# Kernel tuning notes

Measured on AMD Instinct MI355X. Metric: run time of the kernel, lower is better.

## Reference

```python
import jax, jax.numpy as jnp
import numpy as np

B, S, D = 16, 2048, 128

def setup_inputs() -> dict:
    key = jax.random.key(0)
    k1, k2, k3, k4 = jax.random.split(key, 4)
    q = jax.random.normal(k1, (B, S, D), dtype=jnp.float32)
    k = jax.random.normal(k2, (B, S, D), dtype=jnp.float32)
    v = jax.random.normal(k3, (B, S, D), dtype=jnp.float32)
    scale = jnp.float32(1.0 / np.sqrt(D))
    attn_mask = jax.random.randint(k4, (B, S, S), 0, 2).astype(jnp.bool_)
    return {"q": q, "k": k, "v": v, "scale": scale, "attn_mask": attn_mask}

def reference(q, k, v, scale, attn_mask):
    # attention scores: [B, Sq, Sk]
    scores = jnp.einsum('bqd,bkd->bqk', q, k) * scale
    # masked_fill(attn_mask, -inf): True positions are masked out
    scores = jnp.where(attn_mask, -jnp.inf, scores)
    attention = jax.nn.softmax(scores, axis=2)
    # dropout prob = 0.0 -> identity
    context = jnp.einsum('bqk,bkd->bqd', attention, v)
    return (context, attention)
```

## Files before the change

### kernel.cpp

```cpp
#include <hip/hip_runtime.h>
#include <hip/hip_bf16.h>
#include <hip/hip_fp16.h>

#define B_ 16
#define S_ 2048
#define D_ 128
#define QB 64
#define KT 64
#define NT_ 32
#define LOG2E 1.4426950408889634f

typedef __attribute__((ext_vector_type(8))) short short8;
typedef __attribute__((ext_vector_type(4))) float f32x4;
typedef __attribute__((ext_vector_type(4))) float f32x4v;
typedef __attribute__((ext_vector_type(4))) int i32x4;
typedef __attribute__((ext_vector_type(4))) unsigned short u16x4;

__device__ __forceinline__ float exp2fast(float x) {
  return __builtin_amdgcn_exp2f(x);
}
__device__ __forceinline__ unsigned short f2bf(float f) {
  unsigned int u = __builtin_bit_cast(unsigned int, f);
  unsigned int r = (u + 0x7fffu + ((u >> 16) & 1u)) >> 16;
  return (unsigned short)r;
}
__device__ __forceinline__ float bf2f(unsigned short h) {
  return __builtin_bit_cast(float, (unsigned int)h << 16);
}
__device__ __forceinline__ void gl16(const void* g, void* l) {
  __builtin_amdgcn_global_load_lds(
      (const __attribute__((address_space(1))) unsigned int*)g,
      (__attribute__((address_space(3))) unsigned int*)l, 16, 0, 0);
}
__device__ __forceinline__ int swz_bid(int bid, int nwg) {
  int cpx = nwg >> 3;
  return (bid & 7) * cpx + (bid >> 3);
}

__global__ void cvt_bf16_kernel(const float* __restrict__ x,
                                unsigned short* __restrict__ y,
                                const float* __restrict__ sc, float postmul,
                                int n4) {
  int i = blockIdx.x * blockDim.x + threadIdx.x;
  if (i >= n4) return;
  float s = (sc ? sc[0] : 1.0f) * postmul;
  float4 f = reinterpret_cast<const float4*>(x)[i];
  u16x4 o;
  o[0] = f2bf(f.x * s); o[1] = f2bf(f.y * s);
  o[2] = f2bf(f.z * s); o[3] = f2bf(f.w * s);
  reinterpret_cast<u16x4*>(y)[i] = o;
}

__global__ void vtrans_kernel(const float* __restrict__ v,
                              unsigned short* __restrict__ vT) {
  __shared__ float tile[32][33];
  int b = blockIdx.z, kt = blockIdx.x, dt = blockIdx.y;
  int t = threadIdx.x;
  int c = t & 31, r0 = t >> 5;
  const float* src = v + ((size_t)b * S_ + (size_t)kt * 32) * D_ + dt * 32;
#pragma unroll
  for (int i = 0; i < 4; i++) {
    int r = r0 + 8 * i;
    tile[r][c] = src[(size_t)r * D_ + c];
  }
  __syncthreads();
  unsigned short* dst = vT + ((size_t)b * D_ + dt * 32) * S_ + (size_t)kt * 32;
#pragma unroll
  for (int i = 0; i < 4; i++) {
    int r = r0 + 8 * i;
    dst[(size_t)r * S_ + c] = f2bf(tile[c][r]);
  }
}

__global__ __launch_bounds__(512, 4)
void attn_main_kernel(const unsigned short* __restrict__ qbf,
                      const unsigned short* __restrict__ kbf,
                      const unsigned short* __restrict__ vTb,
                      const void* __restrict__ maskp,
                      float* __restrict__ ctx,
                      float* __restrict__ att) {
  __shared__ __align__(16) char kbuf[2][KT * 256];
  __shared__ __align__(16) char vbuf[2][D_ * 128];
  __shared__ __align__(16) char etile[QB * 128];
  __shared__ float zpart[8][2][16];
  __shared__ float iz_l[QB];

  const int tid = threadIdx.x;
  const int bid = swz_bid(blockIdx.x, B_ * (S_ / QB));
  const int b  = bid >> 5;
  const int q0 = (bid & 31) << 6;

  const int w   = tid >> 6;
  const int l   = tid & 63;
  const int l16 = l & 15;
  const int lq  = l >> 4;
  const int qh  = w & 1;
  const int kq  = w >> 1;

  const char* kbb = reinterpret_cast<const char*>(kbf + (((size_t)b * S_) << 7));
  const char* vbb = reinterpret_cast<const char*>(vTb + ((size_t)b * D_) * S_);

  const int krow_g = w * 4 + (l >> 4);
  const size_t ksrc = (size_t)krow_g * 256 + (((l & 15) * 16) ^ ((krow_g & 15) << 4));
  const int vrow_g = w * 8 + (l >> 3);
  const size_t vsrc = (size_t)vrow_g * (S_ * 2) + (((l & 7) * 16) ^ ((vrow_g & 7) << 4));
  const int ldsoff = w * 1024;

  gl16(kbb + ksrc,        &kbuf[0][0] + ldsoff);
  gl16(kbb + ksrc + 8192, &kbuf[0][0] + ldsoff + 8192);

  int myv = 0;
  if (tid < 256) myv = (reinterpret_cast<const unsigned int*>(maskp)[tid] > 1u) ? 1 : 0;
  const int mask_is_byte = __syncthreads_or(myv);

  short8 qf[2][4];
#pragma unroll
  for (int qg = 0; qg < 2; ++qg) {
    const unsigned short* qp =
        qbf + (((size_t)(b * S_ + q0 + qh * 32 + qg * 16 + l16)) << 7) + lq * 8;
#pragma unroll
    for (int ks = 0; ks < 4; ks++)
      qf[qg][ks] = *reinterpret_cast<const short8*>(qp + ks * 32);
  }

  const unsigned char* mask8 = reinterpret_cast<const unsigned char*>(maskp);
  const int* mask32 = reinterpret_cast<const int*>(maskp);
  size_t mrowq[2];
#pragma unroll
  for (int qg = 0; qg < 2; ++qg)
    mrowq[qg] = ((size_t)b * S_ + q0 + qh * 32 + qg * 16 + l16) * S_ + kq * 16 + lq * 4;

  unsigned int mbits[8] = {0, 0, 0, 0, 0, 0, 0, 0};
  float Zl[2] = {0.0f, 0.0f};
  const int krow_f = kq * 16 + l16;
  const int kfx = (krow_f & 15) << 4;

  for (int t = 0; t < NT_; ++t) {
    const int cur = t & 1;
    if (t < NT_ - 1) {
      const char* src = kbb + (size_t)(t + 1) * (KT * 256);
      gl16(src + ksrc,        &kbuf[cur ^ 1][0] + ldsoff);
      gl16(src + ksrc + 8192, &kbuf[cur ^ 1][0] + ldsoff + 8192);
    }
    unsigned int nib[2];
    if (mask_is_byte) {
#pragma unroll
      for (int qg = 0; qg < 2; ++qg) {
        unsigned int mv = *reinterpret_cast<const unsigned int*>(
            mask8 + mrowq[qg] + t * KT);
        nib[qg] = ((mv & 0x000000ffu) ? 1u : 0u) | ((mv & 0x0000ff00u) ? 2u : 0u) |
                  ((mv & 0x00ff0000u) ? 4u : 0u) | ((mv & 0xff000000u) ? 8u : 0u);
      }
    } else {
#pragma unroll
      for (int qg = 0; qg < 2; ++qg) {
        i32x4 mi = *reinterpret_cast<const i32x4*>(mask32 + mrowq[qg] + t * KT);
        nib[qg] = (mi[0] ? 1u : 0u) | (mi[1] ? 2u : 0u) |
                  (mi[2] ? 4u : 0u) | (mi[3] ? 8u : 0u);
      }
    }
    mbits[t >> 2] |= (nib[0] | (nib[1] << 4)) << ((t & 3) * 8);

    const char* kp = &kbuf[cur][0] + krow_f * 256;
    f32x4 a0 = {0.f, 0.f, 0.f, 0.f}, a1 = {0.f, 0.f, 0.f, 0.f};
    __builtin_amdgcn_s_setprio(1);
#pragma unroll
    for (int ks = 0; ks < 4; ++ks) {
      short8 kfr = *reinterpret_cast<const short8*>(kp + ((ks * 64 + lq * 16) ^ kfx));
      a0 = __builtin_amdgcn_mfma_f32_16x16x32_bf16(kfr, qf[0][ks], a0, 0, 0, 0);
      a1 = __builtin_amdgcn_mfma_f32_16x16x32_bf16(kfr, qf[1][ks], a1, 0, 0, 0);
    }
    __builtin_amdgcn_s_setprio(0);
#pragma unroll
    for (int r = 0; r < 4; ++r) {
      if (!((nib[0] >> r) & 1u)) Zl[0] += exp2fast(a0[r]);
      if (!((nib[1] >> r) & 1u)) Zl[1] += exp2fast(a1[r]);
    }
    __syncthreads();
  }

  gl16(kbb + ksrc,          &kbuf[0][0] + ldsoff);
  gl16(kbb + ksrc + 8192,   &kbuf[0][0] + ldsoff + 8192);
  gl16(vbb + vsrc,          &vbuf[0][0] + ldsoff);
  gl16(vbb + vsrc + 262144, &vbuf[0][0] + ldsoff + 8192);
#pragma unroll
  for (int qg = 0; qg < 2; ++qg) {
    Zl[qg] += __shfl_xor(Zl[qg], 16, 64);
    Zl[qg] += __shfl_xor(Zl[qg], 32, 64);
  }
  if (lq == 0) { zpart[w][0][l16] = Zl[0]; zpart[w][1][l16] = Zl[1]; }
  __syncthreads();
  if (tid < QB) {
    const int qh_ = tid >> 5, qg_ = (tid >> 4) & 1, r_ = tid & 15;
    float Z = 0.0f;
#pragma unroll
    for (int kk = 0; kk < 4; ++kk) Z += zpart[kk * 2 + qh_][qg_][r_];
    iz_l[tid] = 1.0f / Z;
  }
  __syncthreads();

  const float izq0 = iz_l[qh * 32 + l16];
  const float izq1 = iz_l[qh * 32 + 16 + l16];

  f32x4 apv[2][2] = {{{0.f,0.f,0.f,0.f},{0.f,0.f,0.f,0.f}},
                     {{0.f,0.f,0.f,0.f},{0.f,0.f,0.f,0.f}}};
  for (int t = 0; t < NT_; ++t) {
    const int cur = t & 1;
    if (t < NT_ - 1) {
      const char* src = kbb + (size_t)(t + 1) * (KT * 256);
      gl16(src + ksrc,        &kbuf[cur ^ 1][0] + ldsoff);
      gl16(src + ksrc + 8192, &kbuf[cur ^ 1][0] + ldsoff + 8192);
    }
    const char* kp = &kbuf[cur][0] + krow_f * 256;
    f32x4 a0 = {0.f, 0.f, 0.f, 0.f}, a1 = {0.f, 0.f, 0.f, 0.f};
    __builtin_amdgcn_s_setprio(1);
#pragma unroll
    for (int ks = 0; ks < 4; ++ks) {
      short8 kfr = *reinterpret_cast<const short8*>(kp + ((ks * 64 + lq * 16) ^ kfx));
      a0 = __builtin_amdgcn_mfma_f32_16x16x32_bf16(kfr, qf[0][ks], a0, 0, 0, 0);
      a1 = __builtin_amdgcn_mfma_f32_16x16x32_bf16(kfr, qf[1][ks], a1, 0, 0, 0);
    }
    __builtin_amdgcn_s_setprio(0);
    const unsigned int nibs = mbits[t >> 2] >> ((t & 3) * 8);
    u16x4 eb[2];
#pragma unroll
    for (int r = 0; r < 4; ++r) {
      eb[0][r] = f2bf((nibs & (1u << r)) ? 0.0f : exp2fast(a0[r]) * izq0);
      eb[1][r] = f2bf((nibs & (16u << r)) ? 0.0f : exp2fast(a1[r]) * izq1);
    }
    __syncthreads();
#pragma unroll
    for (int qg = 0; qg < 2; ++qg) {
      const int re = qh * 32 + qg * 16 + l16;
      *reinterpret_cast<u16x4*>(
          etile + re * 128 + ((kq * 32 + lq * 8) ^ ((re & 7) << 4))) = eb[qg];
    }
    __syncthreads();
#pragma unroll
    for (int h = 0; h < 2; ++h) {
      const int re = w * 8 + h * 4 + (l >> 4);
      u16x4 ev = *reinterpret_cast<const u16x4*>(
          etile + re * 128 + (((l & 15) * 8) ^ ((re & 7) << 4)));
      f32x4v pv;
#pragma unroll
      for (int j = 0; j < 4; ++j) pv[j] = bf2f(ev[j]);
      __builtin_nontemporal_store(pv, reinterpret_cast<f32x4v*>(
          att + ((size_t)(b * S_ + q0 + re)) * S_ + t * KT + (l & 15) * 4));
    }
#pragma unroll
    for (int kk = 0; kk < 2; ++kk) {
      short8 afr[2], bfr[2];
#pragma unroll
      for (int qg = 0; qg < 2; ++qg) {
        const int re = qh * 32 + qg * 16 + l16;
        afr[qg] = *reinterpret_cast<const short8*>(
            etile + re * 128 + ((kk * 64 + lq * 16) ^ ((re & 7) << 4)));
      }
#pragma unroll
      for (int dg = 0; dg < 2; ++dg) {
        const int vr = kq * 32 + dg * 16 + l16;
        bfr[dg] = *reinterpret_cast<const short8*>(
            &vbuf[cur][0] + vr * 128 + ((kk * 64 + lq * 16) ^ ((vr & 7) << 4)));
      }
      __builtin_amdgcn_s_setprio(1);
#pragma unroll
      for (int qg = 0; qg < 2; ++qg)
#pragma unroll
        for (int dg = 0; dg < 2; ++dg)
          apv[qg][dg] = __builtin_amdgcn_mfma_f32_16x16x32_bf16(
              afr[qg], bfr[dg], apv[qg][dg], 0, 0, 0);
      __builtin_amdgcn_s_setprio(0);
    }
    if (t < NT_ - 1) {
      const char* vs2 = vbb + (size_t)(t + 1) * 128;
      gl16(vs2 + vsrc,          &vbuf[cur ^ 1][0] + ldsoff);
      gl16(vs2 + vsrc + 262144, &vbuf[cur ^ 1][0] + ldsoff + 8192);
    }
  }

#pragma unroll
  for (int qg = 0; qg < 2; ++qg) {
#pragma unroll
    for (int dg = 0; dg < 2; ++dg) {
#pragma unroll
      for (int r = 0; r < 4; ++r) {
        __builtin_nontemporal_store(
            apv[qg][dg][r],
            ctx + ((size_t)(b * S_ + q0 + qh * 32 + qg * 16 + lq * 4 + r)) * D_ +
                kq * 32 + dg * 16 + l16);
      }
    }
  }
}

extern "C" void kernel_launch(void* const* d_in, const int* in_sizes, int n_in,
                              void* d_out, int out_size, void* d_ws, size_t ws_size,
                              hipStream_t stream) {
  (void)in_sizes; (void)n_in; (void)out_size; (void)ws_size;
  const float* q = (const float*)d_in[0];
  const float* k = (const float*)d_in[1];
  const float* v = (const float*)d_in[2];
  const float* scale = (const float*)d_in[3];
  const void* mask = d_in[4];

  const size_t qkv_elems = (size_t)B_ * S_ * D_;
  unsigned short* qbf = (unsigned short*)d_ws;
  unsigned short* kbf = qbf + qkv_elems;
  unsigned short* vTb = kbf + qkv_elems;

  float* ctx = (float*)d_out;
  float* att = ctx + (size_t)B_ * S_ * D_;

  const int n4 = B_ * S_ * D_ / 4;
  cvt_bf16_kernel<<<dim3((n4 + 255) / 256), dim3(256), 0, stream>>>(
      q, qbf, scale, LOG2E, n4);
  cvt_bf16_kernel<<<dim3((n4 + 255) / 256), dim3(256), 0, stream>>>(
      k, kbf, nullptr, 1.0f, n4);
  vtrans_kernel<<<dim3(S_ / 32, D_ / 32, B_), dim3(256), 0, stream>>>(v, vTb);
  attn_main_kernel<<<dim3(B_ * (S_ / QB)), dim3(512), 0, stream>>>(
      qbf, kbf, vTb, mask, ctx, att);
}
```

Baseline: 159.9 us.

## Halve key tile to 32 and remap warps for higher occupancy

Shrinks the key tile from 64 to 32 columns, which doubles the iteration count and halves the LDS buffers for K, V and the probability tile. Warps are remapped so each handles 16 query rows and half of the key/D range instead of 32 rows. Launch bounds ask for 8 blocks per CU so more waves can hide latency. The cost is twice as many barriers per pass, less MFMA reuse per K fragment, and narrower mask and attention-output stores per iteration.

Result: slower. 250.3 us (+56.5%).

```diff
diff --git a/kernel.cpp b/kernel.cpp
--- a/kernel.cpp
+++ b/kernel.cpp
@@ -6,8 +6,8 @@
 #define S_ 2048
 #define D_ 128
 #define QB 64
-#define KT 64
-#define NT_ 32
+#define KT 32
+#define NT_ 64
 #define LOG2E 1.4426950408889634f
 
 typedef __attribute__((ext_vector_type(8))) short short8;
@@ -72,7 +72,7 @@
   }
 }
 
-__global__ __launch_bounds__(512, 4)
+__global__ __launch_bounds__(512, 8)
 void attn_main_kernel(const unsigned short* __restrict__ qbf,
                       const unsigned short* __restrict__ kbf,
                       const unsigned short* __restrict__ vTb,
@@ -80,9 +80,9 @@
                       float* __restrict__ ctx,
                       float* __restrict__ att) {
   __shared__ __align__(16) char kbuf[2][KT * 256];
-  __shared__ __align__(16) char vbuf[2][D_ * 128];
-  __shared__ __align__(16) char etile[QB * 128];
-  __shared__ float zpart[8][2][16];
+  __shared__ __align__(16) char vbuf[2][D_ * 64];
+  __shared__ __align__(16) char etile[QB * 64];
+  __shared__ float zpart[8][16];
   __shared__ float iz_l[QB];
 
   const int tid = threadIdx.x;
@@ -94,201 +94,149 @@
   const int l   = tid & 63;
   const int l16 = l & 15;
   const int lq  = l >> 4;
-  const int qh  = w & 1;
-  const int kq  = w >> 1;
+  const int qq  = w >> 1;
+  const int kq  = w & 1;
 
   const char* kbb = reinterpret_cast<const char*>(kbf + (((size_t)b * S_) << 7));
   const char* vbb = reinterpret_cast<const char*>(vTb + ((size_t)b * D_) * S_);
 
-  const int krow_g = w * 4 + (l >> 4);
-  const size_t ksrc = (size_t)krow_g * 256 + (((l & 15) * 16) ^ ((krow_g & 15) << 4));
-  const int vrow_g = w * 8 + (l >> 3);
-  const size_t vsrc = (size_t)vrow_g * (S_ * 2) + (((l & 7) * 16) ^ ((vrow_g & 7) << 4));
+  const int krow_g = tid >> 4;
+  const size_t ksrc = (size_t)krow_g * 256 + (((tid & 15) * 16) ^ ((krow_g & 15) << 4));
+  const int vrow_g = tid >> 2;
+  const size_t vsrc = (size_t)vrow_g * (S_ * 2) + (((tid & 3) * 16) ^ ((vrow_g & 3) << 4));
   const int ldsoff = w * 1024;
 
-  gl16(kbb + ksrc,        &kbuf[0][0] + ldsoff);
-  gl16(kbb + ksrc + 8192, &kbuf[0][0] + ldsoff + 8192);
+  gl16(kbb + ksrc, &kbuf[0][0] + ldsoff);
 
   int myv = 0;
   if (tid < 256) myv = (reinterpret_cast<const unsigned int*>(maskp)[tid] > 1u) ? 1 : 0;
   const int mask_is_byte = __syncthreads_or(myv);
 
-  short8 qf[2][4];
-#pragma unroll
-  for (int qg = 0; qg < 2; ++qg) {
+  short8 qf[4];
+  {
     const unsigned short* qp =
-        qbf + (((size_t)(b * S_ + q0 + qh * 32 + qg * 16 + l16)) << 7) + lq * 8;
+        qbf + (((size_t)(b * S_ + q0 + qq * 16 + l16)) << 7) + lq * 8;
 #pragma unroll
     for (int ks = 0; ks < 4; ks++)
-      qf[qg][ks] = *reinterpret_cast<const short8*>(qp + ks * 32);
+      qf[ks] = *reinterpret_cast<const short8*>(qp + ks * 32);
   }
 
   const unsigned char* mask8 = reinterpret_cast<const unsigned char*>(maskp);
   const int* mask32 = reinterpret_cast<const int*>(maskp);
-  size_t mrowq[2];
-#pragma unroll
-  for (int qg = 0; qg < 2; ++qg)
-    mrowq[qg] = ((size_t)b * S_ + q0 + qh * 32 + qg * 16 + l16) * S_ + kq * 16 + lq * 4;
+  const size_t mrow =
+      ((size_t)b * S_ + q0 + qq * 16 + l16) * S_ + kq * 16 + lq * 4;
 
   unsigned int mbits[8] = {0, 0, 0, 0, 0, 0, 0, 0};
-  float Zl[2] = {0.0f, 0.0f};
+  float Zl = 0.0f;
   const int krow_f = kq * 16 + l16;
   const int kfx = (krow_f & 15) << 4;
 
   for (int t = 0; t < NT_; ++t) {
     const int cur = t & 1;
-    if (t < NT_ - 1) {
-      const char* src = kbb + (size_t)(t + 1) * (KT * 256);
-      gl16(src + ksrc,        &kbuf[cur ^ 1][0] + ldsoff);
-      gl16(src + ksrc + 8192, &kbuf[cur ^ 1][0] + ldsoff + 8192);
-    }
-    unsigned int nib[2];
+    if (t < NT_ - 1)
+      gl16(kbb + (size_t)(t + 1) * (KT * 256) + ksrc, &kbuf[cur ^ 1][0] + ldsoff);
+    unsigned int nib;
     if (mask_is_byte) {
-#pragma unroll
-      for (int qg = 0; qg < 2; ++qg) {
-        unsigned int mv = *reinterpret_cast<const unsigned int*>(
-            mask8 + mrowq[qg] + t * KT);
-        nib[qg] = ((mv & 0x000000ffu) ? 1u : 0u) | ((mv & 0x0000ff00u) ? 2u : 0u) |
-                  ((mv & 0x00ff0000u) ? 4u : 0u) | ((mv & 0xff000000u) ? 8u : 0u);
-      }
+      unsigned int mv = *reinterpret_cast<const unsigned int*>(mask8 + mrow + t * KT);
+      nib = ((mv & 0x000000ffu) ? 1u : 0u) | ((mv & 0x0000ff00u) ? 2u : 0u) |
+            ((mv & 0x00ff0000u) ? 4u : 0u) | ((mv & 0xff000000u) ? 8u : 0u);
     } else {
-#pragma unroll
-      for (int qg = 0; qg < 2; ++qg) {
-        i32x4 mi = *reinterpret_cast<const i32x4*>(mask32 + mrowq[qg] + t * KT);
-        nib[qg] = (mi[0] ? 1u : 0u) | (mi[1] ? 2u : 0u) |
-                  (mi[2] ? 4u : 0u) | (mi[3] ? 8u : 0u);
-      }
-    }
-    mbits[t >> 2] |= (nib[0] | (nib[1] << 4)) << ((t & 3) * 8);
+      i32x4 mi = *reinterpret_cast<const i32x4*>(mask32 + mrow + t * KT);
+      nib = (mi[0] ? 1u : 0u) | (mi[1] ? 2u : 0u) |
+            (mi[2] ? 4u : 0u) | (mi[3] ? 8u : 0u);
+    }
+    mbits[t >> 3] |= nib << ((t & 7) * 4);
 
     const char* kp = &kbuf[cur][0] + krow_f * 256;
-    f32x4 a0 = {0.f, 0.f, 0.f, 0.f}, a1 = {0.f, 0.f, 0.f, 0.f};
+    f32x4 a0 = {0.f, 0.f, 0.f, 0.f};
     __builtin_amdgcn_s_setprio(1);
 #pragma unroll
     for (int ks = 0; ks < 4; ++ks) {
       short8 kfr = *reinterpret_cast<const short8*>(kp + ((ks * 64 + lq * 16) ^ kfx));
-      a0 = __builtin_amdgcn_mfma_f32_16x16x32_bf16(kfr, qf[0][ks], a0, 0, 0, 0);
-      a1 = __builtin_amdgcn_mfma_f32_16x16x32_bf16(kfr, qf[1][ks], a1, 0, 0, 0);
+      a0 = __builtin_amdgcn_mfma_f32_16x16x32_bf16(kfr, qf[ks], a0, 0, 0, 0);
     }
     __builtin_amdgcn_s_setprio(0);
 #pragma unroll
-    for (int r = 0; r < 4; ++r) {
-      if (!((nib[0] >> r) & 1u)) Zl[0] += exp2fast(a0[r]);
-      if (!((nib[1] >> r) & 1u)) Zl[1] += exp2fast(a1[r]);
-    }
+    for (int r = 0; r < 4; ++r)
+      if (!((nib >> r) & 1u)) Zl += exp2fast(a0[r]);
     __syncthreads();
   }
 
-  gl16(kbb + ksrc,          &kbuf[0][0] + ldsoff);
-  gl16(kbb + ksrc + 8192,   &kbuf[0][0] + ldsoff + 8192);
-  gl16(vbb + vsrc,          &vbuf[0][0] + ldsoff);
-  gl16(vbb + vsrc + 262144, &vbuf[0][0] + ldsoff + 8192);
-#pragma unroll
-  for (int qg = 0; qg < 2; ++qg) {
-    Zl[qg] += __shfl_xor(Zl[qg], 16, 64);
-    Zl[qg] += __shfl_xor(Zl[qg], 32, 64);
-  }
-  if (lq == 0) { zpart[w][0][l16] = Zl[0]; zpart[w][1][l16] = Zl[1]; }
+  gl16(kbb + ksrc, &kbuf[0][0] + ldsoff);
+  gl16(vbb + vsrc, &vbuf[0][0] + ldsoff);
+  Zl += __shfl_xor(Zl, 16, 64);
+  Zl += __shfl_xor(Zl, 32, 64);
+  if (lq == 0) zpart[w][l16] = Zl;
   __syncthreads();
   if (tid < QB) {
-    const int qh_ = tid >> 5, qg_ = (tid >> 4) & 1, r_ = tid & 15;
-    float Z = 0.0f;
-#pragma unroll
-    for (int kk = 0; kk < 4; ++kk) Z += zpart[kk * 2 + qh_][qg_][r_];
-    iz_l[tid] = 1.0f / Z;
+    const int qq_ = tid >> 4, r_ = tid & 15;
+    iz_l[tid] = 1.0f / (zpart[qq_ * 2][r_] + zpart[qq_ * 2 + 1][r_]);
   }
   __syncthreads();
 
-  const float izq0 = iz_l[qh * 32 + l16];
-  const float izq1 = iz_l[qh * 32 + 16 + l16];
-
-  f32x4 apv[2][2] = {{{0.f,0.f,0.f,0.f},{0.f,0.f,0.f,0.f}},
-                     {{0.f,0.f,0.f,0.f},{0.f,0.f,0.f,0.f}}};
+  const float izq = iz_l[qq * 16 + l16];
+
+  f32x4 apv[4] = {{0.f,0.f,0.f,0.f},{0.f,0.f,0.f,0.f},
+                  {0.f,0.f,0.f,0.f},{0.f,0.f,0.f,0.f}};
+  const int re2 = qq * 16 + l16;
+  const int e2x = (re2 & 3) << 4;
   for (int t = 0; t < NT_; ++t) {
     const int cur = t & 1;
-    if (t < NT_ - 1) {
-      const char* src = kbb + (size_t)(t + 1) * (KT * 256);
-      gl16(src + ksrc,        &kbuf[cur ^ 1][0] + ldsoff);
-      gl16(src + ksrc + 8192, &kbuf[cur ^ 1][0] + ldsoff + 8192);
-    }
+    if (t < NT_ - 1)
+      gl16(kbb + (size_t)(t + 1) * (KT * 256) + ksrc, &kbuf[cur ^ 1][0] + ldsoff);
     const char* kp = &kbuf[cur][0] + krow_f * 256;
-    f32x4 a0 = {0.f, 0.f, 0.f, 0.f}, a1 = {0.f, 0.f, 0.f, 0.f};
+    f32x4 a0 = {0.f, 0.f, 0.f, 0.f};
     __builtin_amdgcn_s_setprio(1);
 #pragma unroll
     for (int ks = 0; ks < 4; ++ks) {
       short8 kfr = *reinterpret_cast<const short8*>(kp + ((ks * 64 + lq * 16) ^ kfx));
-      a0 = __builtin_amdgcn_mfma_f32_16x16x32_bf16(kfr, qf[0][ks], a0, 0, 0, 0);
-      a1 = __builtin_amdgcn_mfma_f32_16x16x32_bf16(kfr, qf[1][ks], a1, 0, 0, 0);
+      a0 = __builtin_amdgcn_mfma_f32_16x16x32_bf16(kfr, qf[ks], a0, 0, 0, 0);
     }
     __builtin_amdgcn_s_setprio(0);
-    const unsigned int nibs = mbits[t >> 2] >> ((t & 3) * 8);
-    u16x4 eb[2];
-#pragma unroll
-    for (int r = 0; r < 4; ++r) {
-      eb[0][r] = f2bf((nibs & (1u << r)) ? 0.0f : exp2fast(a0[r]) * izq0);
-      eb[1][r] = f2bf((nibs & (16u << r)) ? 0.0f : exp2fast(a1[r]) * izq1);
-    }
+    const unsigned int nib = (mbits[t >> 3] >> ((t & 7) * 4)) & 15u;
+    u16x4 eb;
+#pragma unroll
+    for (int r = 0; r < 4; ++r)
+      eb[r] = f2bf(((nib >> r) & 1u) ? 0.0f : exp2fast(a0[r]) * izq);
     __syncthreads();
-#pragma unroll
-    for (int qg = 0; qg < 2; ++qg) {
-      const int re = qh * 32 + qg * 16 + l16;
-      *reinterpret_cast<u16x4*>(
-          etile + re * 128 + ((kq * 32 + lq * 8) ^ ((re & 7) << 4))) = eb[qg];
-    }
+    *reinterpret_cast<u16x4*>(
+        etile + re2 * 64 + ((kq * 32 + lq * 8) ^ e2x)) = eb;
     __syncthreads();
-#pragma unroll
-    for (int h = 0; h < 2; ++h) {
-      const int re = w * 8 + h * 4 + (l >> 4);
+    {
+      const int ra = w * 8 + (l >> 3);
       u16x4 ev = *reinterpret_cast<const u16x4*>(
-          etile + re * 128 + (((l & 15) * 8) ^ ((re & 7) << 4)));
+          etile + ra * 64 + (((l & 7) * 8) ^ ((ra & 3) << 4)));
       f32x4v pv;
 #pragma unroll
       for (int j = 0; j < 4; ++j) pv[j] = bf2f(ev[j]);
       __builtin_nontemporal_store(pv, reinterpret_cast<f32x4v*>(
-          att + ((size_t)(b * S_ + q0 + re)) * S_ + t * KT + (l & 15) * 4));
-    }
-#pragma unroll
-    for (int kk = 0; kk < 2; ++kk) {
-      short8 afr[2], bfr[2];
-#pragma unroll
-      for (int qg = 0; qg < 2; ++qg) {
-        const int re = qh * 32 + qg * 16 + l16;
-        afr[qg] = *reinterpret_cast<const short8*>(
-            etile + re * 128 + ((kk * 64 + lq * 16) ^ ((re & 7) << 4)));
+          att + ((size_t)(b * S_ + q0 + ra)) * S_ + t * KT + (l & 7) * 4));
+    }
+    {
+      short8 afr = *reinterpret_cast<const short8*>(
+          etile + re2 * 64 + ((lq * 16) ^ e2x));
+      __builtin_amdgcn_s_setprio(1);
+#pragma unroll
+      for (int dg = 0; dg < 4; ++dg) {
+        const int vr = kq * 64 + dg * 16 + l16;
+        short8 bfr = *reinterpret_cast<const short8*>(
+            &vbuf[cur][0] + vr * 64 + ((lq * 16) ^ ((vr & 3) << 4)));
+        apv[dg] = __builtin_amdgcn_mfma_f32_16x16x32_bf16(afr, bfr, apv[dg], 0, 0, 0);
       }
-#pragma unroll
-      for (int dg = 0; dg < 2; ++dg) {
-        const int vr = kq * 32 + dg * 16 + l16;
-        bfr[dg] = *reinterpret_cast<const short8*>(
-            &vbuf[cur][0] + vr * 128 + ((kk * 64 + lq * 16) ^ ((vr & 7) << 4)));
-      }
-      __builtin_amdgcn_s_setprio(1);
-#pragma unroll
-      for (int qg = 0; qg < 2; ++qg)
-#pragma unroll
-        for (int dg = 0; dg < 2; ++dg)
-          apv[qg][dg] = __builtin_amdgcn_mfma_f32_16x16x32_bf16(
-              afr[qg], bfr[dg], apv[qg][dg], 0, 0, 0);
       __builtin_amdgcn_s_setprio(0);
     }
-    if (t < NT_ - 1) {
-      const char* vs2 = vbb + (size_t)(t + 1) * 128;
-      gl16(vs2 + vsrc,          &vbuf[cur ^ 1][0] + ldsoff);
-      gl16(vs2 + vsrc + 262144, &vbuf[cur ^ 1][0] + ldsoff + 8192);
-    }
-  }
-
-#pragma unroll
-  for (int qg = 0; qg < 2; ++qg) {
-#pragma unroll
-    for (int dg = 0; dg < 2; ++dg) {
-#pragma unroll
-      for (int r = 0; r < 4; ++r) {
-        __builtin_nontemporal_store(
-            apv[qg][dg][r],
-            ctx + ((size_t)(b * S_ + q0 + qh * 32 + qg * 16 + lq * 4 + r)) * D_ +
-                kq * 32 + dg * 16 + l16);
-      }
+    if (t < NT_ - 1)
+      gl16(vbb + (size_t)(t + 1) * 64 + vsrc, &vbuf[cur ^ 1][0] + ldsoff);
+  }
+
+#pragma unroll
+  for (int dg = 0; dg < 4; ++dg) {
+#pragma unroll
+    for (int r = 0; r < 4; ++r) {
+      __builtin_nontemporal_store(
+          apv[dg][r],
+          ctx + ((size_t)(b * S_ + q0 + qq * 16 + lq * 4 + r)) * D_ +
+              kq * 64 + dg * 16 + l16);
     }
   }
 }
```

## Triple-buffer K in pass one and hoist all mask loads before the loop

Applied to the files above, without the earlier changes.

All mask bits are now loaded and packed into registers up front, before the first QK pass, so the per-tile mask loads leave that pass. The first pass switches from double to triple buffering of K tiles, prefetching two tiles ahead and using an explicit vmcnt wait plus a raw s_barrier instead of __syncthreads. The shared buffers are merged into one pool so the pass-two K/V buffers and etile alias the three K buffers. This aims to hide global latency in the Z pass, at the cost of a burst of mask loads up front and more outstanding memory operations.

New measurement: 169.0 us. 5.7% more time.

```diff
diff --git a/kernel.cpp b/kernel.cpp
--- a/kernel.cpp
+++ b/kernel.cpp
@@ -79,9 +79,7 @@
                       const void* __restrict__ maskp,
                       float* __restrict__ ctx,
                       float* __restrict__ att) {
-  __shared__ __align__(16) char kbuf[2][KT * 256];
-  __shared__ __align__(16) char vbuf[2][D_ * 128];
-  __shared__ __align__(16) char etile[QB * 128];
+  __shared__ __align__(16) char pool[73728];
   __shared__ float zpart[8][2][16];
   __shared__ float iz_l[QB];
 
@@ -106,8 +104,10 @@
   const size_t vsrc = (size_t)vrow_g * (S_ * 2) + (((l & 7) * 16) ^ ((vrow_g & 7) << 4));
   const int ldsoff = w * 1024;
 
-  gl16(kbb + ksrc,        &kbuf[0][0] + ldsoff);
-  gl16(kbb + ksrc + 8192, &kbuf[0][0] + ldsoff + 8192);
+  gl16(kbb + ksrc,                   pool + 0 * 16384 + ldsoff);
+  gl16(kbb + ksrc + 8192,            pool + 0 * 16384 + ldsoff + 8192);
+  gl16(kbb + KT * 256 + ksrc,        pool + 1 * 16384 + ldsoff);
+  gl16(kbb + KT * 256 + ksrc + 8192, pool + 1 * 16384 + ldsoff + 8192);
 
   int myv = 0;
   if (tid < 256) myv = (reinterpret_cast<const unsigned int*>(maskp)[tid] > 1u) ? 1 : 0;
@@ -131,37 +131,44 @@
     mrowq[qg] = ((size_t)b * S_ + q0 + qh * 32 + qg * 16 + l16) * S_ + kq * 16 + lq * 4;
 
   unsigned int mbits[8] = {0, 0, 0, 0, 0, 0, 0, 0};
+  if (mask_is_byte) {
+#pragma unroll
+    for (int t = 0; t < NT_; ++t) {
+      unsigned int m0 = *reinterpret_cast<const unsigned int*>(mask8 + mrowq[0] + t * KT);
+      unsigned int m1 = *reinterpret_cast<const unsigned int*>(mask8 + mrowq[1] + t * KT);
+      unsigned int n0 = ((m0 & 0x000000ffu) ? 1u : 0u) | ((m0 & 0x0000ff00u) ? 2u : 0u) |
+                        ((m0 & 0x00ff0000u) ? 4u : 0u) | ((m0 & 0xff000000u) ? 8u : 0u);
+      unsigned int n1 = ((m1 & 0x000000ffu) ? 1u : 0u) | ((m1 & 0x0000ff00u) ? 2u : 0u) |
+                        ((m1 & 0x00ff0000u) ? 4u : 0u) | ((m1 & 0xff000000u) ? 8u : 0u);
+      mbits[t >> 2] |= (n0 | (n1 << 4)) << ((t & 3) * 8);
+    }
+  } else {
+#pragma unroll
+    for (int t = 0; t < NT_; ++t) {
+      i32x4 m0 = *reinterpret_cast<const i32x4*>(mask32 + mrowq[0] + t * KT);
+      i32x4 m1 = *reinterpret_cast<const i32x4*>(mask32 + mrowq[1] + t * KT);
+      unsigned int n0 = (m0[0] ? 1u : 0u) | (m0[1] ? 2u : 0u) |
+                        (m0[2] ? 4u : 0u) | (m0[3] ? 8u : 0u);
+      unsigned int n1 = (m1[0] ? 1u : 0u) | (m1[1] ? 2u : 0u) |
+                        (m1[2] ? 4u : 0u) | (m1[3] ? 8u : 0u);
+      mbits[t >> 2] |= (n0 | (n1 << 4)) << ((t & 3) * 8);
+    }
+  }
+
   float Zl[2] = {0.0f, 0.0f};
   const int krow_f = kq * 16 + l16;
   const int kfx = (krow_f & 15) << 4;
 
+  char* kb0 = pool + 0 * 16384;
+  char* kb1 = pool + 1 * 16384;
+  char* kb2 = pool + 2 * 16384;
   for (int t = 0; t < NT_; ++t) {
-    const int cur = t & 1;
-    if (t < NT_ - 1) {
-      const char* src = kbb + (size_t)(t + 1) * (KT * 256);
-      gl16(src + ksrc,        &kbuf[cur ^ 1][0] + ldsoff);
-      gl16(src + ksrc + 8192, &kbuf[cur ^ 1][0] + ldsoff + 8192);
-    }
-    unsigned int nib[2];
-    if (mask_is_byte) {
-#pragma unroll
-      for (int qg = 0; qg < 2; ++qg) {
-        unsigned int mv = *reinterpret_cast<const unsigned int*>(
-            mask8 + mrowq[qg] + t * KT);
-        nib[qg] = ((mv & 0x000000ffu) ? 1u : 0u) | ((mv & 0x0000ff00u) ? 2u : 0u) |
-                  ((mv & 0x00ff0000u) ? 4u : 0u) | ((mv & 0xff000000u) ? 8u : 0u);
-      }
-    } else {
-#pragma unroll
-      for (int qg = 0; qg < 2; ++qg) {
-        i32x4 mi = *reinterpret_cast<const i32x4*>(mask32 + mrowq[qg] + t * KT);
-        nib[qg] = (mi[0] ? 1u : 0u) | (mi[1] ? 2u : 0u) |
-                  (mi[2] ? 4u : 0u) | (mi[3] ? 8u : 0u);
-      }
-    }
-    mbits[t >> 2] |= (nib[0] | (nib[1] << 4)) << ((t & 3) * 8);
-
-    const char* kp = &kbuf[cur][0] + krow_f * 256;
+    if (t + 2 < NT_) {
+      const char* src = kbb + (size_t)(t + 2) * (KT * 256);
+      gl16(src + ksrc,        kb2 + ldsoff);
+      gl16(src + ksrc + 8192, kb2 + ldsoff + 8192);
+    }
+    const char* kp = kb0 + krow_f * 256;
     f32x4 a0 = {0.f, 0.f, 0.f, 0.f}, a1 = {0.f, 0.f, 0.f, 0.f};
     __builtin_amdgcn_s_setprio(1);
 #pragma unroll
@@ -171,18 +178,26 @@
       a1 = __builtin_amdgcn_mfma_f32_16x16x32_bf16(kfr, qf[1][ks], a1, 0, 0, 0);
     }
     __builtin_amdgcn_s_setprio(0);
+    const unsigned int nibs = mbits[t >> 2] >> ((t & 3) * 8);
 #pragma unroll
     for (int r = 0; r < 4; ++r) {
-      if (!((nib[0] >> r) & 1u)) Zl[0] += exp2fast(a0[r]);
-      if (!((nib[1] >> r) & 1u)) Zl[1] += exp2fast(a1[r]);
-    }
-    __syncthreads();
-  }
-
-  gl16(kbb + ksrc,          &kbuf[0][0] + ldsoff);
-  gl16(kbb + ksrc + 8192,   &kbuf[0][0] + ldsoff + 8192);
-  gl16(vbb + vsrc,          &vbuf[0][0] + ldsoff);
-  gl16(vbb + vsrc + 262144, &vbuf[0][0] + ldsoff + 8192);
+      if (!(nibs & (1u << r)))  Zl[0] += exp2fast(a0[r]);
+      if (!(nibs & (16u << r))) Zl[1] += exp2fast(a1[r]);
+    }
+    if (t + 2 < NT_) {
+      asm volatile("s_waitcnt vmcnt(2) lgkmcnt(0)" ::: "memory");
+    } else {
+      asm volatile("s_waitcnt vmcnt(0) lgkmcnt(0)" ::: "memory");
+    }
+    __builtin_amdgcn_s_barrier();
+    __builtin_amdgcn_sched_barrier(0);
+    char* tmp = kb0; kb0 = kb1; kb1 = kb2; kb2 = tmp;
+  }
+
+  gl16(kbb + ksrc,          pool + ldsoff);
+  gl16(kbb + ksrc + 8192,   pool + ldsoff + 8192);
+  gl16(vbb + vsrc,          pool + 32768 + ldsoff);
+  gl16(vbb + vsrc + 262144, pool + 32768 + ldsoff + 8192);
 #pragma unroll
   for (int qg = 0; qg < 2; ++qg) {
     Zl[qg] += __shfl_xor(Zl[qg], 16, 64);
@@ -202,16 +217,21 @@
   const float izq0 = iz_l[qh * 32 + l16];
   const float izq1 = iz_l[qh * 32 + 16 + l16];
 
+  char* etile = pool + 65536;
   f32x4 apv[2][2] = {{{0.f,0.f,0.f,0.f},{0.f,0.f,0.f,0.f}},
                      {{0.f,0.f,0.f,0.f},{0.f,0.f,0.f,0.f}}};
   for (int t = 0; t < NT_; ++t) {
     const int cur = t & 1;
+    char* kcur = pool + cur * 16384;
+    char* knxt = pool + (cur ^ 1) * 16384;
+    char* vcur = pool + 32768 + cur * 16384;
+    char* vnxt = pool + 32768 + (cur ^ 1) * 16384;
     if (t < NT_ - 1) {
       const char* src = kbb + (size_t)(t + 1) * (KT * 256);
-      gl16(src + ksrc,        &kbuf[cur ^ 1][0] + ldsoff);
-      gl16(src + ksrc + 8192, &kbuf[cur ^ 1][0] + ldsoff + 8192);
-    }
-    const char* kp = &kbuf[cur][0] + krow_f * 256;
+      gl16(src + ksrc,        knxt + ldsoff);
+      gl16(src + ksrc + 8192, knxt + ldsoff + 8192);
+    }
+    const char* kp = kcur + krow_f * 256;
     f32x4 a0 = {0.f, 0.f, 0.f, 0.f}, a1 = {0.f, 0.f, 0.f, 0.f};
     __builtin_amdgcn_s_setprio(1);
 #pragma unroll
@@ -260,7 +280,7 @@
       for (int dg = 0; dg < 2; ++dg) {
         const int vr = kq * 32 + dg * 16 + l16;
         bfr[dg] = *reinterpret_cast<const short8*>(
-            &vbuf[cur][0] + vr * 128 + ((kk * 64 + lq * 16) ^ ((vr & 7) << 4)));
+            vcur + vr * 128 + ((kk * 64 + lq * 16) ^ ((vr & 7) << 4)));
       }
       __builtin_amdgcn_s_setprio(1);
 #pragma unroll
@@ -273,8 +293,8 @@
     }
     if (t < NT_ - 1) {
       const char* vs2 = vbb + (size_t)(t + 1) * 128;
-      gl16(vs2 + vsrc,          &vbuf[cur ^ 1][0] + ldsoff);
-      gl16(vs2 + vsrc + 262144, &vbuf[cur ^ 1][0] + ldsoff + 8192);
+      gl16(vs2 + vsrc,          vnxt + ldsoff);
+      gl16(vs2 + vsrc + 262144, vnxt + ldsoff + 8192);
     }
   }
 
```
